# Kernel tuning notes

Measured on AMD Instinct MI355X. Metric: run time of the kernel, lower is better.

Reference implementation:

```python
import jax, jax.numpy as jnp
import numpy as np

N, E, Q = 50000, 500000, 100000
IN_DIM, HID, EDGE_DIM, NUM_CLASSES = 128, 128, 16, 2


def _glorot(key, shape):
    fan_in, fan_out = shape
    lim = (6.0 / (fan_in + fan_out)) ** 0.5
    return jax.random.uniform(key, shape, jnp.float32, -lim, lim)


def setup_inputs() -> dict:
    key = jax.random.key(0)
    ks = jax.random.split(key, 12)
    return {
        "node_feature": jax.random.normal(ks[0], (N, IN_DIM), jnp.float32),
        "edge_index": jax.random.randint(ks[1], (2, E), 0, N, jnp.int64),
        "edge_feature": jax.random.normal(ks[2], (E, EDGE_DIM), jnp.float32),
        "edge_label_index": jax.random.randint(ks[3], (2, Q), 0, N, jnp.int64),
        # conv1 params
        "c1_pre_W": _glorot(ks[4], (IN_DIM, IN_DIM)),
        "c1_pre_b": jnp.zeros((IN_DIM,), jnp.float32),
        "c1_msg_W": _glorot(ks[5], (2 * IN_DIM + EDGE_DIM, HID)),
        "c1_msg_b": jnp.zeros((HID,), jnp.float32),
        # conv2 params
        "c2_pre_W": _glorot(ks[6], (HID, HID)),
        "c2_pre_b": jnp.zeros((HID,), jnp.float32),
        "c2_msg_W": _glorot(ks[7], (2 * HID + EDGE_DIM, HID)),
        "c2_msg_b": jnp.zeros((HID,), jnp.float32),
        # link-prediction head
        "lp_W": _glorot(ks[8], (2 * HID, NUM_CLASSES)),
        "lp_b": jnp.zeros((NUM_CLASSES,), jnp.float32),
    }


def _mlp_message_conv(x, edge_index, edge_feature, pre_W, pre_b, msg_W, msg_b):
    # pre_conv: Linear + ReLU
    h = jax.nn.relu(x @ pre_W + pre_b)
    src, dst = edge_index[0], edge_index[1]
    # PyG default flow source_to_target: x_i = target, x_j = source
    x_i = h[dst]  # [E, d]
    x_j = h[src]  # [E, d]
    msg = jnp.concatenate([x_i, x_j, edge_feature], axis=1) @ msg_W + msg_b  # [E, out]
    # aggr='add' onto target nodes
    return jax.ops.segment_sum(msg, dst, num_segments=x.shape[0])


def reference(node_feature, edge_index, edge_feature, edge_label_index,
              c1_pre_W, c1_pre_b, c1_msg_W, c1_msg_b,
              c2_pre_W, c2_pre_b, c2_msg_W, c2_msg_b,
              lp_W, lp_b):
    # eval mode: dropout is identity
    x = jax.nn.relu(_mlp_message_conv(node_feature, edge_index, edge_feature,
                                      c1_pre_W, c1_pre_b, c1_msg_W, c1_msg_b))
    x = _mlp_message_conv(x, edge_index, edge_feature,
                          c2_pre_W, c2_pre_b, c2_msg_W, c2_msg_b)
    nodes_first = x[edge_label_index[0]]   # [Q, hid]
    nodes_second = x[edge_label_index[1]]  # [Q, hid]
    pred = jnp.concatenate([nodes_first, nodes_second], axis=-1) @ lp_W + lp_b
    return pred
```

## Files before the change

kernel.cpp:

```cpp
#include <hip/hip_runtime.h>
#include <cstdint>
#include <cstddef>


typedef __attribute__((ext_vector_type(8))) short short8;
typedef __attribute__((ext_vector_type(4))) float float4v;

__device__ __forceinline__ ushort f2b(float f) {
    uint u = __float_as_uint(f);
    u = u + 0x7fff + ((u >> 16) & 1);
    return (ushort)(u >> 16);
}
__device__ __forceinline__ float b2f(ushort h) {
    return __uint_as_float(((uint)h) << 16);
}
__device__ __forceinline__ uint pack2(float a, float b) {
    return (uint)f2b(a) | ((uint)f2b(b) << 16);
}

__device__ __forceinline__ void gload16(const void* gsrc, void* ldst) {
    __builtin_amdgcn_global_load_lds(
        (const __attribute__((address_space(1))) void*)gsrc,
        (__attribute__((address_space(3))) void*)ldst, 16, 0, 0);
}

#define F_MSG     1
#define F_RELU    2
#define F_DEGBIAS 4
#define F_OUTB    8
#define F_IN32    16
#define F_HEAD    32

__launch_bounds__(256, 3)
__global__ void gemm_mfma(const ushort* __restrict__ A, const ushort* __restrict__ B,
                          const ushort* __restrict__ EF, const float* __restrict__ A32,
                          const float* __restrict__ DEG, const ushort* __restrict__ Wt,
                          const float* __restrict__ bias, ushort* __restrict__ outB,
                          ushort* __restrict__ outD,
                          const float* __restrict__ lpW, float* __restrict__ z,
                          int M, int Kp, int flags)
{
    __shared__ ushort xs[128 * 64];
    __shared__ ushort ws[128 * 64];
    const int tid  = threadIdx.x;
    const int lane = tid & 63;
    const int wave = tid >> 6;
    const int row0 = blockIdx.x << 7;

    float4v acc[2][8];
#pragma unroll
    for (int m = 0; m < 2; ++m)
#pragma unroll
        for (int t = 0; t < 8; ++t) acc[m][t] = (float4v){0.f, 0.f, 0.f, 0.f};

    const int ar0   = (wave << 5) + (lane & 15);
    const int bcol  = lane & 15;
    const int cxor  = lane & 7;
    const int koffc = lane >> 4;
    const int sw16  = (((lane & 7) ^ (lane >> 3)) << 4);

    for (int kt = 0; kt < Kp; kt += 64) {
        const int tix = kt >> 6;
        __syncthreads();
#pragma unroll
        for (int i = 0; i < 4; ++i) {
            const int wsoff = (wave << 11) + (i << 9);
            gload16((const char*)Wt + (((size_t)((tix << 13) + wsoff)) << 1) + (lane << 4),
                    &ws[wsoff]);
        }
        if (flags & F_IN32) {
            for (int idx = tid; idx < 128 * 8; idx += 256) {
                const int r  = idx >> 3;
                const int ch = idx & 7;
                const int gr = row0 + r;
                uint4 v = make_uint4(0, 0, 0, 0);
                if (gr < M) {
                    const float4 f0 = *(const float4*)&A32[((size_t)gr << 7) + kt + (ch << 3)];
                    const float4 f1 = *(const float4*)&A32[((size_t)gr << 7) + kt + (ch << 3) + 4];
                    v.x = pack2(f0.x, f0.y); v.y = pack2(f0.z, f0.w);
                    v.z = pack2(f1.x, f1.y); v.w = pack2(f1.z, f1.w);
                }
                *(uint4*)&xs[(r << 6) + ((ch ^ (r & 7)) << 3)] = v;
            }
        } else {
            const char* srcB; size_t strideB; int toffB;
            if (flags & F_MSG) {
                if (tix < 2)      { srcB = (const char*)A;  strideB = 256; toffB = (tix & 1) << 7; }
                else if (tix < 4) { srcB = (const char*)B;  strideB = 256; toffB = (tix & 1) << 7; }
                else              { srcB = (const char*)EF; strideB = 128; toffB = 0; }
            } else {
                srcB = (const char*)A; strideB = 256; toffB = (tix & 1) << 7;
            }
            const int rb = wave << 5;
#pragma unroll
            for (int i = 0; i < 4; ++i) {
                const int gr = min(row0 + rb + (i << 3) + (lane >> 3), M - 1);
                gload16(srcB + (size_t)gr * strideB + toffB + sw16,
                        &xs[(rb + (i << 3)) << 6]);
            }
        }
        __syncthreads();
#pragma unroll
        for (int sc = 0; sc < 8; sc += 4) {
            const int ra = (sc + koffc) ^ cxor;
            const short8 a0 = *(const short8*)&xs[(ar0 << 6) + (ra << 3)];
            const short8 a1 = *(const short8*)&xs[((ar0 + 16) << 6) + (ra << 3)];
#pragma unroll
            for (int t = 0; t < 8; ++t) {
                const short8 bf = *(const short8*)&ws[(((t << 4) + bcol) << 6) + (ra << 3)];
                acc[0][t] = __builtin_amdgcn_mfma_f32_16x16x32_bf16(a0, bf, acc[0][t], 0, 0, 0);
                acc[1][t] = __builtin_amdgcn_mfma_f32_16x16x32_bf16(a1, bf, acc[1][t], 0, 0, 0);
            }
        }
    }

    float bcv[8];
#pragma unroll
    for (int t = 0; t < 8; ++t) bcv[t] = bias[(t << 4) + bcol];

    if (flags & F_HEAD) {
        const float2* lw = (const float2*)lpW;
        float2 wa[8], wb[8];
#pragma unroll
        for (int t = 0; t < 8; ++t) {
            const int col = (t << 4) + bcol;
            wa[t] = lw[col];
            wb[t] = lw[128 + col];
        }
#pragma unroll
        for (int m = 0; m < 2; ++m) {
            const int rbase = row0 + (wave << 5) + (m << 4) + ((lane >> 4) << 2);
#pragma unroll
            for (int r = 0; r < 4; ++r) {
                const int row = rbase + r;
                const float d = (row < M) ? DEG[row] : 0.f;
                float za0 = 0.f, za1 = 0.f, zb0 = 0.f, zb1 = 0.f;
#pragma unroll
                for (int t = 0; t < 8; ++t) {
                    const float v = acc[m][t][r] + d * bcv[t];
                    za0 += v * wa[t].x; za1 += v * wa[t].y;
                    zb0 += v * wb[t].x; zb1 += v * wb[t].y;
                }
#pragma unroll
                for (int mk = 8; mk > 0; mk >>= 1) {
                    za0 += __shfl_xor(za0, mk);
                    za1 += __shfl_xor(za1, mk);
                    zb0 += __shfl_xor(zb0, mk);
                    zb1 += __shfl_xor(zb1, mk);
                }
                if (bcol == 0 && row < M)
                    *(float4*)&z[(size_t)row * 4] = make_float4(za0, za1, zb0, zb1);
            }
        }
    } else {
#pragma unroll
        for (int m = 0; m < 2; ++m) {
            const int rbase = row0 + (wave << 5) + (m << 4) + ((lane >> 4) << 2);
#pragma unroll
            for (int r = 0; r < 4; ++r) {
                const int row = rbase + r;
                if (row >= M) continue;
                const float d = DEG[row];
#pragma unroll
                for (int t = 0; t < 8; ++t) {
                    const int col = (t << 4) + bcol;
                    float v = acc[m][t][r];
                    v += (flags & F_DEGBIAS) ? d * bcv[t] : bcv[t];
                    if (flags & F_RELU) v = fmaxf(v, 0.f);
                    outB[((size_t)row << 7) + col] = f2b(v);
                    if (outD) outD[((size_t)row << 7) + col] = f2b(v * d);
                }
            }
        }
    }
}

__launch_bounds__(256)
__global__ void prep(const float* __restrict__ c1pW, const float* __restrict__ c2pW,
                     const float* __restrict__ c1mW, const float* __restrict__ c2mW,
                     ushort* __restrict__ wtp1, ushort* __restrict__ wtp2,
                     ushort* __restrict__ wtm1, ushort* __restrict__ wtm2,
                     ushort* __restrict__ efp, int* __restrict__ counts, int N)
{
    const int gtid = blockIdx.x * 256 + threadIdx.x;
    const int gstr = gridDim.x * 256;
    for (int i = gtid; i < N; i += gstr) counts[i] = 0;
    for (int i = gtid; i < N * 8; i += gstr)
        ((uint4*)efp)[i] = make_uint4(0, 0, 0, 0);
    for (int idx = gtid; idx < 2 * 128 * 64; idx += gstr) {
        const int s = idx & 63, n = (idx >> 6) & 127, t = idx >> 13;
        const int k = t * 64 + (((s >> 3) ^ (n & 7)) << 3) + (s & 7);
        wtp1[idx] = f2b(c1pW[(size_t)k * 128 + n]);
        wtp2[idx] = f2b(c2pW[(size_t)k * 128 + n]);
    }
    for (int idx = gtid; idx < 5 * 128 * 64; idx += gstr) {
        const int s = idx & 63, n = (idx >> 6) & 127, t = idx >> 13;
        const int k = t * 64 + (((s >> 3) ^ (n & 7)) << 3) + (s & 7);
        wtm1[idx] = (k < 272) ? f2b(c1mW[(size_t)k * 128 + n]) : (ushort)0;
        wtm2[idx] = (k < 272) ? f2b(c2mW[(size_t)k * 128 + n]) : (ushort)0;
    }
}

__launch_bounds__(256)
__global__ void hist_kernel(const int* __restrict__ ei, int* __restrict__ counts, int E)
{
    const int e = blockIdx.x * 256 + threadIdx.x;
    if (e < E) atomicAdd(&counts[ei[E + e]], 1);
}

__launch_bounds__(256)
__global__ void scan_phase1(const int* __restrict__ counts, int* __restrict__ rowstart,
                            int* __restrict__ blocksums, int N)
{
    __shared__ int sdata[256];
    const int t = threadIdx.x;
    const int i = blockIdx.x * 256 + t;
    const int v = (i < N) ? counts[i] : 0;
    sdata[t] = v;
    __syncthreads();
    for (int off = 1; off < 256; off <<= 1) {
        const int add = (t >= off) ? sdata[t - off] : 0;
        __syncthreads();
        sdata[t] += add;
        __syncthreads();
    }
    if (i < N) rowstart[i] = sdata[t] - v;
    if (t == 255) blocksums[blockIdx.x] = sdata[255];
}

__launch_bounds__(256)
__global__ void scan_phase23(const int* __restrict__ counts, const int* __restrict__ bs,
                             int* __restrict__ rowstart, int* __restrict__ cursor,
                             float* __restrict__ degf, int N, int E)
{
    __shared__ int sdata[256];
    const int t = threadIdx.x;
    const int vb = blockIdx.x;
    int part = 0;
    for (int j = t; j < vb; j += 256) part += bs[j];
    sdata[t] = part;
    __syncthreads();
    for (int s = 128; s > 0; s >>= 1) {
        if (t < s) sdata[t] += sdata[t + s];
        __syncthreads();
    }
    const int off = sdata[0];
    const int i = vb * 256 + t;
    if (i < N) {
        const int rs = rowstart[i] + off;
        rowstart[i] = rs;
        cursor[i]   = rs;
        degf[i]     = (float)counts[i];
    }
    if (vb == 0 && t == 0) rowstart[N] = E;
}

__launch_bounds__(256)
__global__ void build_elist(const int* __restrict__ ei, int* __restrict__ cursor,
                            int2* __restrict__ elist, int E)
{
    const int e = blockIdx.x * 256 + threadIdx.x;
    if (e >= E) return;
    const int d = ei[E + e];
    const int pos = atomicAdd(&cursor[d], 1);
    elist[pos] = make_int2(ei[e], e);
}

__launch_bounds__(256)
__global__ void gather(const int2* __restrict__ elist, const int* __restrict__ rowstart,
                       const ushort* __restrict__ h, ushort* __restrict__ agg,
                       const float* __restrict__ ef, ushort* __restrict__ aggef,
                       int N, int doEf)
{
    const int tid = threadIdx.x;
    const int grp = tid >> 4;
    const int l   = tid & 15;
    const int nvb = (N + 15) / 16;
    for (int vb = blockIdx.x; vb < nvb; vb += gridDim.x) {
        const int node = vb * 16 + grp;
        if (node >= N) continue;
        const int beg = rowstart[node];
        const int end = rowstart[node + 1];
        float a0 = 0.f, a1 = 0.f, a2 = 0.f, a3 = 0.f;
        float a4 = 0.f, a5 = 0.f, a6 = 0.f, a7 = 0.f;
        float efacc = 0.f;
        int k = beg;
        while (k < end) {
            const int cnt = min(16, end - k);
            const int2 ep = elist[k + min(l, cnt - 1)];
            int j = 0;
            for (; j + 8 <= cnt; j += 8) {
                uint4 v[8];
                float efv[8];
#pragma unroll
                for (int jj = 0; jj < 8; ++jj) {
                    const int s = __shfl(ep.x, j + jj, 16);
                    v[jj] = *(const uint4*)&h[((size_t)s << 7) + (l << 3)];
                    if (doEf) {
                        const int y = __shfl(ep.y, j + jj, 16);
                        efv[jj] = ef[((size_t)y << 4) + l];
                    }
                }
#pragma unroll
                for (int jj = 0; jj < 8; ++jj) {
                    a0 += b2f((ushort)(v[jj].x & 0xffff));
                    a1 += b2f((ushort)(v[jj].x >> 16));
                    a2 += b2f((ushort)(v[jj].y & 0xffff));
                    a3 += b2f((ushort)(v[jj].y >> 16));
                    a4 += b2f((ushort)(v[jj].z & 0xffff));
                    a5 += b2f((ushort)(v[jj].z >> 16));
                    a6 += b2f((ushort)(v[jj].w & 0xffff));
                    a7 += b2f((ushort)(v[jj].w >> 16));
                    if (doEf) efacc += efv[jj];
                }
            }
            for (; j < cnt; ++j) {
                const int s = __shfl(ep.x, j, 16);
                const uint4 v = *(const uint4*)&h[((size_t)s << 7) + (l << 3)];
                if (doEf) {
                    const int y = __shfl(ep.y, j, 16);
                    efacc += ef[((size_t)y << 4) + l];
                }
                a0 += b2f((ushort)(v.x & 0xffff));
                a1 += b2f((ushort)(v.x >> 16));
                a2 += b2f((ushort)(v.y & 0xffff));
                a3 += b2f((ushort)(v.y >> 16));
                a4 += b2f((ushort)(v.z & 0xffff));
                a5 += b2f((ushort)(v.z >> 16));
                a6 += b2f((ushort)(v.w & 0xffff));
                a7 += b2f((ushort)(v.w >> 16));
            }
            k += cnt;
        }
        uint4 o;
        o.x = pack2(a0, a1);
        o.y = pack2(a2, a3);
        o.z = pack2(a4, a5);
        o.w = pack2(a6, a7);
        *(uint4*)&agg[((size_t)node << 7) + (l << 3)] = o;
        if (doEf) aggef[((size_t)node << 6) + l] = f2b(efacc);
    }
}

__launch_bounds__(256)
__global__ void head_kernel(const float4* __restrict__ z, const int* __restrict__ eli,
                            const float* __restrict__ lpb, float* __restrict__ out, int Q)
{
    const int q = blockIdx.x * 256 + threadIdx.x;
    if (q >= Q) return;
    const int a = eli[q];
    const int b = eli[Q + q];
    const float4 za = z[a];
    const float4 zb = z[b];
    float2 o = make_float2(za.x + zb.z + lpb[0], za.y + zb.w + lpb[1]);
    *(float2*)&out[(size_t)q * 2] = o;
}

extern "C" void kernel_launch(void* const* d_in, const int* in_sizes, int n_in,
                              void* d_out, int out_size, void* d_ws, size_t ws_size,
                              hipStream_t stream)
{
    const float* nf   = (const float*)d_in[0];
    const int*   ei   = (const int*)d_in[1];
    const float* ef   = (const float*)d_in[2];
    const int*   eli  = (const int*)d_in[3];
    const float* c1pW = (const float*)d_in[4];
    const float* c1pb = (const float*)d_in[5];
    const float* c1mW = (const float*)d_in[6];
    const float* c1mb = (const float*)d_in[7];
    const float* c2pW = (const float*)d_in[8];
    const float* c2pb = (const float*)d_in[9];
    const float* c2mW = (const float*)d_in[10];
    const float* c2mb = (const float*)d_in[11];
    const float* lpW  = (const float*)d_in[12];
    const float* lpb  = (const float*)d_in[13];
    float* out = (float*)d_out;

    const int N = in_sizes[0] / 128;
    const int E = in_sizes[1] / 2;
    const int Q = in_sizes[3] / 2;

    float* DEG = (float*)d_ws;
    float* z   = DEG + N;
    int* counts    = (int*)(z + (size_t)N * 4);
    int* rowstart  = counts + N;
    int* cursor    = rowstart + N + 1;
    int* blocksums = cursor + N;
    uintptr_t ep8 = (uintptr_t)(blocksums + 1024);
    ep8 = (ep8 + 7) & ~(uintptr_t)7;
    int2* elist = (int2*)ep8;
    uintptr_t up = (uintptr_t)(elist + E);
    up = (up + 15) & ~(uintptr_t)15;
    ushort* h_bf   = (ushort*)up;
    ushort* agg_bf = h_bf   + (size_t)N * 128;
    ushort* x1_bf  = agg_bf + (size_t)N * 128;
    ushort* hd_bf  = x1_bf  + (size_t)N * 128;
    ushort* efp    = hd_bf  + (size_t)N * 128;
    ushort* wtp1   = efp    + (size_t)N * 64;
    ushort* wtm1   = wtp1 + 2 * 128 * 64;
    ushort* wtp2   = wtm1 + 5 * 128 * 64;
    ushort* wtm2   = wtp2 + 2 * 128 * 64;

    const int gemmGrid = (N + 127) / 128;
    const int eGrid    = (E + 255) / 256;
    const int nGrid    = (N + 255) / 256;
    const int gGrid    = (N + 15) / 16;
    const int headGrid = (Q + 255) / 256;

    prep<<<nGrid, 256, 0, stream>>>(c1pW, c2pW, c1mW, c2mW, wtp1, wtp2, wtm1, wtm2,
                                    efp, counts, N);
    hist_kernel<<<eGrid, 256, 0, stream>>>(ei, counts, E);
    scan_phase1<<<nGrid, 256, 0, stream>>>(counts, rowstart, blocksums, N);
    scan_phase23<<<nGrid, 256, 0, stream>>>(counts, blocksums, rowstart, cursor, DEG, N, E);
    build_elist<<<eGrid, 256, 0, stream>>>(ei, cursor, elist, E);

    gemm_mfma<<<gemmGrid, 256, 0, stream>>>(nullptr, nullptr, nullptr, nf, DEG, wtp1,
                                            c1pb, h_bf, hd_bf, nullptr, nullptr, N, 128,
                                            F_RELU | F_OUTB | F_IN32);
    gather<<<gGrid, 256, 0, stream>>>(elist, rowstart, h_bf, agg_bf, ef, efp, N, 1);
    gemm_mfma<<<gemmGrid, 256, 0, stream>>>(hd_bf, agg_bf, efp, nullptr, DEG, wtm1,
                                            c1mb, x1_bf, nullptr, nullptr, nullptr, N, 320,
                                            F_MSG | F_RELU | F_DEGBIAS | F_OUTB);

    gemm_mfma<<<gemmGrid, 256, 0, stream>>>(x1_bf, nullptr, nullptr, nullptr, DEG, wtp2,
                                            c2pb, h_bf, hd_bf, nullptr, nullptr, N, 128,
                                            F_RELU | F_OUTB);
    gather<<<gGrid, 256, 0, stream>>>(elist, rowstart, h_bf, agg_bf, nullptr, nullptr, N, 0);
    gemm_mfma<<<gemmGrid, 256, 0, stream>>>(hd_bf, agg_bf, efp, nullptr, DEG, wtm2,
                                            c2mb, nullptr, nullptr, lpW, z, N, 320,
                                            F_MSG | F_DEGBIAS | F_HEAD);

    head_kernel<<<headGrid, 256, 0, stream>>>((const float4*)z, eli, lpb, out, Q);
}
```

Before: 291.8 us.

## Fuse conv1 message GEMM with conv2 pre-linear and pre-convert node features

Adds a gemm_msg_pre kernel that computes the conv1 message GEMM, keeps the ReLU'd x1 tile in shared memory, and immediately applies conv2's pre-linear. This removes one launch and the x1 round trip through global memory. The fp32 node-feature conversion moves into prep, so the first GEMM can use the async global-to-LDS bf16 load path. The gather tail loop is folded into the 8-wide unrolled loop with masked entries, which adds redundant loads for partial groups. The fused kernel uses 48KB of shared memory, which may lower occupancy, and it writes hd_bf in place while reading it, which is safe only because each block touches its own rows.

Measured after the change: 286.2 us. Within noise of the previous version (-1.9%).

```diff
diff --git a/kernel.cpp b/kernel.cpp
--- a/kernel.cpp
+++ b/kernel.cpp
@@ -28,12 +28,11 @@
 #define F_RELU    2
 #define F_DEGBIAS 4
 #define F_OUTB    8
-#define F_IN32    16
 #define F_HEAD    32
 
 __launch_bounds__(256, 3)
 __global__ void gemm_mfma(const ushort* __restrict__ A, const ushort* __restrict__ B,
-                          const ushort* __restrict__ EF, const float* __restrict__ A32,
+                          const ushort* __restrict__ EF,
                           const float* __restrict__ DEG, const ushort* __restrict__ Wt,
                           const float* __restrict__ bias, ushort* __restrict__ outB,
                           ushort* __restrict__ outD,
@@ -68,21 +67,7 @@
             gload16((const char*)Wt + (((size_t)((tix << 13) + wsoff)) << 1) + (lane << 4),
                     &ws[wsoff]);
         }
-        if (flags & F_IN32) {
-            for (int idx = tid; idx < 128 * 8; idx += 256) {
-                const int r  = idx >> 3;
-                const int ch = idx & 7;
-                const int gr = row0 + r;
-                uint4 v = make_uint4(0, 0, 0, 0);
-                if (gr < M) {
-                    const float4 f0 = *(const float4*)&A32[((size_t)gr << 7) + kt + (ch << 3)];
-                    const float4 f1 = *(const float4*)&A32[((size_t)gr << 7) + kt + (ch << 3) + 4];
-                    v.x = pack2(f0.x, f0.y); v.y = pack2(f0.z, f0.w);
-                    v.z = pack2(f1.x, f1.y); v.w = pack2(f1.z, f1.w);
-                }
-                *(uint4*)&xs[(r << 6) + ((ch ^ (r & 7)) << 3)] = v;
-            }
-        } else {
+        {
             const char* srcB; size_t strideB; int toffB;
             if (flags & F_MSG) {
                 if (tix < 2)      { srcB = (const char*)A;  strideB = 256; toffB = (tix & 1) << 7; }
@@ -175,8 +160,148 @@
     }
 }
 
-__launch_bounds__(256)
-__global__ void prep(const float* __restrict__ c1pW, const float* __restrict__ c2pW,
+__launch_bounds__(256, 3)
+__global__ void gemm_msg_pre(const ushort* __restrict__ HD, const ushort* __restrict__ AGG,
+                             const ushort* __restrict__ EFP, const float* __restrict__ DEG,
+                             const ushort* __restrict__ Wm, const float* __restrict__ bm,
+                             const ushort* __restrict__ Wp, const float* __restrict__ bp,
+                             ushort* __restrict__ outH, ushort* __restrict__ outHD, int M)
+{
+    __shared__ ushort smem[128 * 128 + 128 * 64];
+    ushort* x2 = smem;
+    ushort* ws = smem + 128 * 128;
+
+    const int tid  = threadIdx.x;
+    const int lane = tid & 63;
+    const int wave = tid >> 6;
+    const int row0 = blockIdx.x << 7;
+
+    float4v acc[2][8];
+#pragma unroll
+    for (int m = 0; m < 2; ++m)
+#pragma unroll
+        for (int t = 0; t < 8; ++t) acc[m][t] = (float4v){0.f, 0.f, 0.f, 0.f};
+
+    const int ar0   = (wave << 5) + (lane & 15);
+    const int bcol  = lane & 15;
+    const int cxor  = lane & 7;
+    const int koffc = lane >> 4;
+    const int sw16  = (((lane & 7) ^ (lane >> 3)) << 4);
+
+    for (int kt = 0; kt < 320; kt += 64) {
+        const int tix = kt >> 6;
+        __syncthreads();
+#pragma unroll
+        for (int i = 0; i < 4; ++i) {
+            const int wsoff = (wave << 11) + (i << 9);
+            gload16((const char*)Wm + (((size_t)((tix << 13) + wsoff)) << 1) + (lane << 4),
+                    &ws[wsoff]);
+        }
+        {
+            const char* srcB; size_t strideB; int toffB;
+            if (tix < 2)      { srcB = (const char*)HD;  strideB = 256; toffB = (tix & 1) << 7; }
+            else if (tix < 4) { srcB = (const char*)AGG; strideB = 256; toffB = (tix & 1) << 7; }
+            else              { srcB = (const char*)EFP; strideB = 128; toffB = 0; }
+            const int rb = wave << 5;
+#pragma unroll
+            for (int i = 0; i < 4; ++i) {
+                const int gr = min(row0 + rb + (i << 3) + (lane >> 3), M - 1);
+                gload16(srcB + (size_t)gr * strideB + toffB + sw16,
+                        &smem[(rb + (i << 3)) << 6]);
+            }
+        }
+        __syncthreads();
+#pragma unroll
+        for (int sc = 0; sc < 8; sc += 4) {
+            const int ra = (sc + koffc) ^ cxor;
+            const short8 a0 = *(const short8*)&smem[(ar0 << 6) + (ra << 3)];
+            const short8 a1 = *(const short8*)&smem[((ar0 + 16) << 6) + (ra << 3)];
+#pragma unroll
+            for (int t = 0; t < 8; ++t) {
+                const short8 bf = *(const short8*)&ws[(((t << 4) + bcol) << 6) + (ra << 3)];
+                acc[0][t] = __builtin_amdgcn_mfma_f32_16x16x32_bf16(a0, bf, acc[0][t], 0, 0, 0);
+                acc[1][t] = __builtin_amdgcn_mfma_f32_16x16x32_bf16(a1, bf, acc[1][t], 0, 0, 0);
+            }
+        }
+    }
+
+    float bcv1[8];
+#pragma unroll
+    for (int t = 0; t < 8; ++t) bcv1[t] = bm[(t << 4) + bcol];
+
+    __syncthreads();
+#pragma unroll
+    for (int m = 0; m < 2; ++m) {
+        const int rl0 = (wave << 5) + (m << 4) + ((lane >> 4) << 2);
+#pragma unroll
+        for (int r = 0; r < 4; ++r) {
+            const int rl  = rl0 + r;
+            const int row = row0 + rl;
+            const float d = (row < M) ? DEG[row] : 0.f;
+#pragma unroll
+            for (int t = 0; t < 8; ++t) {
+                const int col = (t << 4) + bcol;
+                const float v = fmaxf(acc[m][t][r] + d * bcv1[t], 0.f);
+                const int ch = col >> 3;
+                const int st = (ch & 8) | ((ch ^ rl) & 7);
+                x2[(rl << 7) + (st << 3) + (col & 7)] = f2b(v);
+            }
+        }
+    }
+
+#pragma unroll
+    for (int m = 0; m < 2; ++m)
+#pragma unroll
+        for (int t = 0; t < 8; ++t) acc[m][t] = (float4v){0.f, 0.f, 0.f, 0.f};
+
+    for (int kt2 = 0; kt2 < 2; ++kt2) {
+        __syncthreads();
+#pragma unroll
+        for (int i = 0; i < 4; ++i) {
+            const int wsoff = (wave << 11) + (i << 9);
+            gload16((const char*)Wp + (((size_t)((kt2 << 13) + wsoff)) << 1) + (lane << 4),
+                    &ws[wsoff]);
+        }
+        __syncthreads();
+#pragma unroll
+        for (int sc = 0; sc < 8; sc += 4) {
+            const int ra = (sc + koffc) ^ cxor;
+            const short8 a0 = *(const short8*)&x2[(ar0 << 7) + (kt2 << 6) + (ra << 3)];
+            const short8 a1 = *(const short8*)&x2[((ar0 + 16) << 7) + (kt2 << 6) + (ra << 3)];
+#pragma unroll
+            for (int t = 0; t < 8; ++t) {
+                const short8 bf = *(const short8*)&ws[(((t << 4) + bcol) << 6) + (ra << 3)];
+                acc[0][t] = __builtin_amdgcn_mfma_f32_16x16x32_bf16(a0, bf, acc[0][t], 0, 0, 0);
+                acc[1][t] = __builtin_amdgcn_mfma_f32_16x16x32_bf16(a1, bf, acc[1][t], 0, 0, 0);
+            }
+        }
+    }
+
+    float bcv2[8];
+#pragma unroll
+    for (int t = 0; t < 8; ++t) bcv2[t] = bp[(t << 4) + bcol];
+#pragma unroll
+    for (int m = 0; m < 2; ++m) {
+        const int rbase = row0 + (wave << 5) + (m << 4) + ((lane >> 4) << 2);
+#pragma unroll
+        for (int r = 0; r < 4; ++r) {
+            const int row = rbase + r;
+            if (row >= M) continue;
+            const float d = DEG[row];
+#pragma unroll
+            for (int t = 0; t < 8; ++t) {
+                const int col = (t << 4) + bcol;
+                const float v = fmaxf(acc[m][t][r] + bcv2[t], 0.f);
+                outH[((size_t)row << 7) + col]  = f2b(v);
+                outHD[((size_t)row << 7) + col] = f2b(v * d);
+            }
+        }
+    }
+}
+
+__launch_bounds__(256)
+__global__ void prep(const float* __restrict__ nf, ushort* __restrict__ nf_bf,
+                     const float* __restrict__ c1pW, const float* __restrict__ c2pW,
                      const float* __restrict__ c1mW, const float* __restrict__ c2mW,
                      ushort* __restrict__ wtp1, ushort* __restrict__ wtp2,
                      ushort* __restrict__ wtm1, ushort* __restrict__ wtm2,
@@ -185,6 +310,14 @@
     const int gtid = blockIdx.x * 256 + threadIdx.x;
     const int gstr = gridDim.x * 256;
     for (int i = gtid; i < N; i += gstr) counts[i] = 0;
+    for (int i = gtid; i < N * 16; i += gstr) {
+        const float4 f0 = *(const float4*)&nf[(size_t)i * 8];
+        const float4 f1 = *(const float4*)&nf[(size_t)i * 8 + 4];
+        uint4 v;
+        v.x = pack2(f0.x, f0.y); v.y = pack2(f0.z, f0.w);
+        v.z = pack2(f1.x, f1.y); v.w = pack2(f1.z, f1.w);
+        ((uint4*)nf_bf)[i] = v;
+    }
     for (int i = gtid; i < N * 8; i += gstr)
         ((uint4*)efp)[i] = make_uint4(0, 0, 0, 0);
     for (int idx = gtid; idx < 2 * 128 * 64; idx += gstr) {
@@ -284,25 +417,28 @@
         float a0 = 0.f, a1 = 0.f, a2 = 0.f, a3 = 0.f;
         float a4 = 0.f, a5 = 0.f, a6 = 0.f, a7 = 0.f;
         float efacc = 0.f;
-        int k = beg;
-        while (k < end) {
+        for (int k = beg; k < end; k += 16) {
             const int cnt = min(16, end - k);
             const int2 ep = elist[k + min(l, cnt - 1)];
-            int j = 0;
-            for (; j + 8 <= cnt; j += 8) {
+            for (int j = 0; j < cnt; j += 8) {
                 uint4 v[8];
                 float efv[8];
 #pragma unroll
                 for (int jj = 0; jj < 8; ++jj) {
-                    const int s = __shfl(ep.x, j + jj, 16);
+                    const int idx = min(j + jj, cnt - 1);
+                    const int s = __shfl(ep.x, idx, 16);
                     v[jj] = *(const uint4*)&h[((size_t)s << 7) + (l << 3)];
                     if (doEf) {
-                        const int y = __shfl(ep.y, j + jj, 16);
+                        const int y = __shfl(ep.y, idx, 16);
                         efv[jj] = ef[((size_t)y << 4) + l];
                     }
                 }
 #pragma unroll
                 for (int jj = 0; jj < 8; ++jj) {
+                    if (j + jj >= cnt) {
+                        v[jj] = make_uint4(0, 0, 0, 0);
+                        efv[jj] = 0.f;
+                    }
                     a0 += b2f((ushort)(v[jj].x & 0xffff));
                     a1 += b2f((ushort)(v[jj].x >> 16));
                     a2 += b2f((ushort)(v[jj].y & 0xffff));
@@ -314,23 +450,6 @@
                     if (doEf) efacc += efv[jj];
                 }
             }
-            for (; j < cnt; ++j) {
-                const int s = __shfl(ep.x, j, 16);
-                const uint4 v = *(const uint4*)&h[((size_t)s << 7) + (l << 3)];
-                if (doEf) {
-                    const int y = __shfl(ep.y, j, 16);
-                    efacc += ef[((size_t)y << 4) + l];
-                }
-                a0 += b2f((ushort)(v.x & 0xffff));
-                a1 += b2f((ushort)(v.x >> 16));
-                a2 += b2f((ushort)(v.y & 0xffff));
-                a3 += b2f((ushort)(v.y >> 16));
-                a4 += b2f((ushort)(v.z & 0xffff));
-                a5 += b2f((ushort)(v.z >> 16));
-                a6 += b2f((ushort)(v.w & 0xffff));
-                a7 += b2f((ushort)(v.w >> 16));
-            }
-            k += cnt;
         }
         uint4 o;
         o.x = pack2(a0, a1);
@@ -391,10 +510,10 @@
     int2* elist = (int2*)ep8;
     uintptr_t up = (uintptr_t)(elist + E);
     up = (up + 15) & ~(uintptr_t)15;
-    ushort* h_bf   = (ushort*)up;
+    ushort* nf_bf  = (ushort*)up;
+    ushort* h_bf   = nf_bf  + (size_t)N * 128;
     ushort* agg_bf = h_bf   + (size_t)N * 128;
-    ushort* x1_bf  = agg_bf + (size_t)N * 128;
-    ushort* hd_bf  = x1_bf  + (size_t)N * 128;
+    ushort* hd_bf  = agg_bf + (size_t)N * 128;
     ushort* efp    = hd_bf  + (size_t)N * 128;
     ushort* wtp1   = efp    + (size_t)N * 64;
     ushort* wtm1   = wtp1 + 2 * 128 * 64;
@@ -407,26 +526,23 @@
     const int gGrid    = (N + 15) / 16;
     const int headGrid = (Q + 255) / 256;
 
-    prep<<<nGrid, 256, 0, stream>>>(c1pW, c2pW, c1mW, c2mW, wtp1, wtp2, wtm1, wtm2,
-                                    efp, counts, N);
+    prep<<<nGrid, 256, 0, stream>>>(nf, nf_bf, c1pW, c2pW, c1mW, c2mW,
+                                    wtp1, wtp2, wtm1, wtm2, efp, counts, N);
     hist_kernel<<<eGrid, 256, 0, stream>>>(ei, counts, E);
     scan_phase1<<<nGrid, 256, 0, stream>>>(counts, rowstart, blocksums, N);
     scan_phase23<<<nGrid, 256, 0, stream>>>(counts, blocksums, rowstart, cursor, DEG, N, E);
     build_elist<<<eGrid, 256, 0, stream>>>(ei, cursor, elist, E);
 
-    gemm_mfma<<<gemmGrid, 256, 0, stream>>>(nullptr, nullptr, nullptr, nf, DEG, wtp1,
+    gemm_mfma<<<gemmGrid, 256, 0, stream>>>(nf_bf, nullptr, nullptr, DEG, wtp1,
                                             c1pb, h_bf, hd_bf, nullptr, nullptr, N, 128,
-                                            F_RELU | F_OUTB | F_IN32);
+                                            F_RELU | F_OUTB);
     gather<<<gGrid, 256, 0, stream>>>(elist, rowstart, h_bf, agg_bf, ef, efp, N, 1);
-    gemm_mfma<<<gemmGrid, 256, 0, stream>>>(hd_bf, agg_bf, efp, nullptr, DEG, wtm1,
-                                            c1mb, x1_bf, nullptr, nullptr, nullptr, N, 320,
-                                            F_MSG | F_RELU | F_DEGBIAS | F_OUTB);
-
-    gemm_mfma<<<gemmGrid, 256, 0, stream>>>(x1_bf, nullptr, nullptr, nullptr, DEG, wtp2,
-                                            c2pb, h_bf, hd_bf, nullptr, nullptr, N, 128,
-                                            F_RELU | F_OUTB);
+
+    gemm_msg_pre<<<gemmGrid, 256, 0, stream>>>(hd_bf, agg_bf, efp, DEG, wtm1, c1mb,
+                                               wtp2, c2pb, h_bf, hd_bf, N);
+
     gather<<<gGrid, 256, 0, stream>>>(elist, rowstart, h_bf, agg_bf, nullptr, nullptr, N, 0);
-    gemm_mfma<<<gemmGrid, 256, 0, stream>>>(hd_bf, agg_bf, efp, nullptr, DEG, wtm2,
+    gemm_mfma<<<gemmGrid, 256, 0, stream>>>(hd_bf, agg_bf, efp, DEG, wtm2,
                                             c2mb, nullptr, nullptr, lpW, z, N, 320,
                                             F_MSG | F_DEGBIAS | F_HEAD);
 
```
